# Kernel optimization log

Hardware: AMD Instinct MI355X
Metric: run time of the kernel (lower is better)

Reference implementation:

```python
import jax, jax.numpy as jnp
import numpy as np

Q, N, H, C, L = 512, 1000, 1024, 128, 8  # questions, students, hidden, concepts, lstm layers
LAM, GUESS = 10.0, 0.25  # self.l and guess_prob


def setup_inputs() -> dict:
    key = jax.random.key(0)
    ks = jax.random.split(key, 12)
    def w(k, shape, fan):
        return (jax.random.uniform(k, shape, jnp.float32, -1.0, 1.0) / np.sqrt(fan)).astype(jnp.float32)
    return {
        "inputs": jax.random.normal(ks[0], (Q, N), jnp.float32),
        "concept_col": jax.random.randint(ks[1], (Q,), 0, C),  # concepts[1][i]
        "W_inp": w(ks[2], (H, N), N),
        "b_inp": jnp.zeros((H,), jnp.float32),
        "W_ih0": w(ks[3], (4 * N, H), H),
        "W_hh0": w(ks[4], (4 * N, N), N),
        "b_ih0": jnp.zeros((4 * N,), jnp.float32),
        "b_hh0": jnp.zeros((4 * N,), jnp.float32),
        "W_ih": w(ks[5], (L - 1, 4 * N, N), N),
        "W_hh": w(ks[6], (L - 1, 4 * N, N), N),
        "b_ih": jnp.zeros((L - 1, 4 * N), jnp.float32),
        "b_hh": jnp.zeros((L - 1, 4 * N), jnp.float32),
        "W_lin": w(ks[7], (C,), 1),  # Linear(1, C) weight, shape [C]
        "b_lin": jnp.zeros((C,), jnp.float32),
        "D_nz": 0.1 * jax.random.normal(ks[8], (Q,), jnp.float32),  # D[concepts]
    }


def _cell(Wih, Whh, bih, bhh, x, h, c):
    # PyTorch LSTM cell, gate order i,f,g,o
    g = Wih @ x + bih + Whh @ h + bhh
    i, f, gg, o = jnp.split(g, 4)
    i, f, o = jax.nn.sigmoid(i), jax.nn.sigmoid(f), jax.nn.sigmoid(o)
    c = f * c + i * jnp.tanh(gg)
    return o * jnp.tanh(c), c


def _forward(inputs, concept_col, W_inp, b_inp, W_ih0, W_hh0, b_ih0, b_hh0,
             W_ih, W_hh, b_ih, b_hh, W_lin, b_lin, D_nz):
    def step(carry, xs):
        h, c, ssum = carry  # h,c: [L,N]
        x_row, cc, d = xs
        x = W_inp @ x_row + b_inp  # [H]
        hs, cs = [], []
        hl, cl = _cell(W_ih0, W_hh0, b_ih0, b_hh0, x, h[0], c[0])
        hs.append(hl); cs.append(cl)
        for l in range(L - 1):
            hl, cl = _cell(W_ih[l], W_hh[l], b_ih[l], b_hh[l], hl, h[l + 1], c[l + 1])
            hs.append(hl); cs.append(cl)
        skills = hl[:, None] * W_lin[None, :] + b_lin  # [N, C]
        skills = (skills - skills.min()) / (skills.max() - skills.min())  # global min-max
        out = jnp.maximum(GUESS, 1.0 - jnp.exp(-LAM * (skills[:, cc] - d)))  # floored_exp_irf, [N]
        return (jnp.stack(hs), jnp.stack(cs), ssum + skills), out

    h0 = jnp.zeros((L, N), inputs.dtype)
    c0 = jnp.zeros((L, N), inputs.dtype)
    s0 = jnp.zeros((N, C), inputs.dtype)
    (h, c, ssum), outputs = jax.lax.scan(step, (h0, c0, s0), (inputs, concept_col, D_nz))
    return outputs, ssum / Q  # outputs [Q,N], averaged skills [N,C]


def reference(inputs, concept_col, W_inp, b_inp, W_ih0, W_hh0, b_ih0, b_hh0,
              W_ih, W_hh, b_ih, b_hh, W_lin, b_lin, D_nz):
    return _forward(inputs, concept_col, W_inp, b_inp, W_ih0, W_hh0, b_ih0, b_hh0,
                    W_ih, W_hh, b_ih, b_hh, W_lin, b_lin, D_nz)
```

## Files before the change

kernel.cpp:

```cpp
#include <hip/hip_runtime.h>
#include <math.h>

#define QQ 512
#define NN 1000
#define HHID 1024
#define HPAD 1024
#define CCON 128
#define G4 4000
#define LAYERS 8
#define TC 64
#define CHUNKS (QQ / TC)
#define CONC 4
#define LBLK 63

__device__ inline float wred_min(float v){ for(int o=32;o;o>>=1) v=fminf(v,__shfl_xor(v,o)); return v; }
__device__ inline float wred_max(float v){ for(int o=32;o;o>>=1) v=fmaxf(v,__shfl_xor(v,o)); return v; }
__device__ inline float wred_sum(float v){ for(int o=32;o;o>>=1) v+=__shfl_xor(v,o); return v; }

__global__ __launch_bounds__(256) void gemm_nt(
    const float* __restrict__ A, const float* __restrict__ B,
    const float* __restrict__ bias1,
    float* __restrict__ C, int M, int K, int R, int lda, int ldc) {
  __shared__ float As[16][65];
  __shared__ float Bs[16][65];
  int tid = threadIdx.x;
  int tx = tid & 15, ty = tid >> 4;
  int m0 = blockIdx.y * 64, r0 = blockIdx.x * 64;
  float acc[4][4] = {};
  for (int k0 = 0; k0 < K; k0 += 16) {
#pragma unroll
    for (int i = 0; i < 4; i++) {
      int idx = tid + 256 * i;
      int ml = idx >> 4, kl = idx & 15;
      int m = m0 + ml, k = k0 + kl;
      As[kl][ml] = (m < M && k < K) ? A[(size_t)m * lda + k] : 0.f;
      int r = r0 + ml;
      Bs[kl][ml] = (r < R && k < K) ? B[(size_t)r * K + k] : 0.f;
    }
    __syncthreads();
#pragma unroll
    for (int kk = 0; kk < 16; kk++) {
      float a[4], b[4];
#pragma unroll
      for (int i = 0; i < 4; i++) a[i] = As[kk][ty * 4 + i];
#pragma unroll
      for (int j = 0; j < 4; j++) b[j] = Bs[kk][tx * 4 + j];
#pragma unroll
      for (int i = 0; i < 4; i++)
#pragma unroll
        for (int j = 0; j < 4; j++) acc[i][j] += a[i] * b[j];
    }
    __syncthreads();
  }
#pragma unroll
  for (int i = 0; i < 4; i++) {
    int m = m0 + ty * 4 + i;
    if (m >= M) continue;
#pragma unroll
    for (int j = 0; j < 4; j++) {
      int r = r0 + tx * 4 + j;
      if (r >= R) continue;
      float v = acc[i][j];
      if (bias1) v += bias1[r];
      C[(size_t)m * ldc + r] = v;
    }
  }
}

struct RPair { const float* Hin; const float* Wih; const float* b1;
               const float* b2; const float* Whh; float* Hout; int* flag;
               float* Call; int t0; int kin; };
struct RArgs { RPair p[CONC]; };

__global__ __launch_bounds__(1024, 4) void lstm_stage(RArgs args) {
  RPair rp = args.p[blockIdx.y];
  __shared__ __align__(16) float As[64][68];
  __shared__ __align__(16) float Bs[64][68];
  __shared__ float gl[TC * 64];
  __shared__ float hs[1024];
  __shared__ int go[TC];
  int tid = threadIdx.x;
  int wave = tid >> 6, lane = tid & 63;
  int n = blockIdx.x * 16 + wave;
  bool active = (n < NN);
  int kin = rp.kin;
  int t0 = rp.t0;

  if (tid >= NN) hs[tid] = 0.f;
  if (tid < TC) go[tid] = 0;

  {
    int tt = tid >> 4;
    int w16 = tid & 15;
    int nn = blockIdx.x * 16 + w16;
    float accq[4] = {0.f, 0.f, 0.f, 0.f};
    float pbq[4];
#pragma unroll
    for (int q = 0; q < 4; q++)
      pbq[q] = (nn < NN) ? rp.b1[q * NN + nn] + rp.b2[q * NN + nn] : 0.f;
    for (int k0 = 0; k0 < kin; k0 += 64) {
#pragma unroll
      for (int i = 0; i < 4; i++) {
        int idx = tid + i * 1024;
        int r = idx >> 6, kk = idx & 63;
        int k = k0 + kk;
        As[r][kk] = (k < kin) ? rp.Hin[(size_t)(t0 + r) * HPAD + k] : 0.f;
        int q = r >> 4, nb = blockIdx.x * 16 + (r & 15);
        Bs[r][kk] = (nb < NN && k < kin)
                        ? rp.Wih[(size_t)(q * NN + nb) * kin + k] : 0.f;
      }
      __syncthreads();
#pragma unroll
      for (int kk = 0; kk < 64; kk += 4) {
        float4 av = *(const float4*)&As[tt][kk];
#pragma unroll
        for (int q = 0; q < 4; q++) {
          float4 bv = *(const float4*)&Bs[q * 16 + w16][kk];
          accq[q] += av.x * bv.x + av.y * bv.y + av.z * bv.z + av.w * bv.w;
        }
      }
      __syncthreads();
    }
#pragma unroll
    for (int q = 0; q < 4; q++)
      gl[tt * 64 + q * 16 + w16] = accq[q] + pbq[q];
  }

  float wreg[4][16];
  if (active) {
#pragma unroll
    for (int q = 0; q < 4; q++) {
      const float* wr = rp.Whh + (size_t)(q * NN + n) * NN;
#pragma unroll
      for (int it = 0; it < 16; it++) {
        int k = it * 64 + lane;
        wreg[q][it] = (k < NN) ? wr[k] : 0.f;
      }
    }
  } else {
#pragma unroll
    for (int q = 0; q < 4; q++)
#pragma unroll
      for (int it = 0; it < 16; it++) wreg[q][it] = 0.f;
  }
#pragma unroll
  for (int q = 0; q < 4; q++)
#pragma unroll
    for (int it = 0; it < 16; it++)
      asm volatile("" : "+v"(wreg[q][it]));

  __syncthreads();

  float creg = 0.f;
  if (t0 > 0 && active) creg = rp.Call[n];

  for (int tt = 0; tt < TC; tt++) {
    int t = t0 + tt;
    if (t > 0) {
      if (wave == 0) {
        for (;;) {
          int v = t;
          if (lane < LBLK)
            v = __hip_atomic_load(&rp.flag[lane], __ATOMIC_RELAXED,
                                  __HIP_MEMORY_SCOPE_AGENT);
          if (__all(v >= t)) break;
          __builtin_amdgcn_s_sleep(2);
        }
        if (lane == 0)
          __hip_atomic_store(&go[tt], 1, __ATOMIC_RELAXED,
                             __HIP_MEMORY_SCOPE_WORKGROUP);
      } else {
        while (__hip_atomic_load(&go[tt], __ATOMIC_RELAXED,
                                 __HIP_MEMORY_SCOPE_WORKGROUP) == 0)
          __builtin_amdgcn_s_sleep(1);
      }
      if (tid < NN)
        hs[tid] = __hip_atomic_load(&rp.Hout[(size_t)(t - 1) * HPAD + tid],
                                    __ATOMIC_RELAXED, __HIP_MEMORY_SCOPE_AGENT);
      __syncthreads();
    }
    if (active) {
      float g0 = gl[tt * 64 + wave];
      float g1 = gl[tt * 64 + 16 + wave];
      float g2 = gl[tt * 64 + 32 + wave];
      float g3 = gl[tt * 64 + 48 + wave];
      if (t > 0) {
        float a0 = 0.f, a1 = 0.f, a2 = 0.f, a3 = 0.f;
#pragma unroll
        for (int it = 0; it < 16; it++) {
          float hv = hs[it * 64 + lane];
          a0 += wreg[0][it] * hv;
          a1 += wreg[1][it] * hv;
          a2 += wreg[2][it] * hv;
          a3 += wreg[3][it] * hv;
        }
#pragma unroll
        for (int o = 32; o; o >>= 1) {
          a0 += __shfl_xor(a0, o);
          a1 += __shfl_xor(a1, o);
          a2 += __shfl_xor(a2, o);
          a3 += __shfl_xor(a3, o);
        }
        g0 += a0; g1 += a1; g2 += a2; g3 += a3;
      }
      float ii = 1.f / (1.f + expf(-g0));
      float ff = 1.f / (1.f + expf(-g1));
      float gg = tanhf(g2);
      float oo = 1.f / (1.f + expf(-g3));
      creg = ff * creg + ii * gg;
      float h = oo * tanhf(creg);
      if (lane == 0)
        __hip_atomic_store(&rp.Hout[(size_t)t * HPAD + n], h, __ATOMIC_RELAXED,
                           __HIP_MEMORY_SCOPE_AGENT);
    }
    asm volatile("s_waitcnt vmcnt(0)" ::: "memory");
    __syncthreads();
    if (tid == 0)
      __hip_atomic_store(&rp.flag[blockIdx.x], t + 1, __ATOMIC_RELAXED,
                         __HIP_MEMORY_SCOPE_AGENT);
  }
  if (active && lane == 0)
    __hip_atomic_store(&rp.Call[n], creg, __ATOMIC_RELAXED,
                       __HIP_MEMORY_SCOPE_AGENT);
}

__global__ __launch_bounds__(256) void epilogue_out(
    const float* __restrict__ H7,
    const float* __restrict__ Wlin, const float* __restrict__ blin,
    const int* __restrict__ ccol, const float* __restrict__ Dnz,
    float* __restrict__ out,
    float* __restrict__ irbuf, float* __restrict__ mnirbuf) {
  int t = blockIdx.x, tid = threadIdx.x;
  int wave = tid >> 6, lane = tid & 63;
  __shared__ float hbuf[NN];
  __shared__ float smin[4], smax[4];
  __shared__ float bc[2];
  float lmin = 3.4e38f, lmax = -3.4e38f;
  for (int i = tid; i < NN; i += 256) {
    float v = H7[(size_t)t * HPAD + i];
    hbuf[i] = v;
    lmin = fminf(lmin, v); lmax = fmaxf(lmax, v);
  }
  lmin = wred_min(lmin); lmax = wred_max(lmax);
  if (lane == 0) { smin[wave] = lmin; smax[wave] = lmax; }
  __syncthreads();
  if (tid == 0) {
    bc[0] = fminf(fminf(smin[0], smin[1]), fminf(smin[2], smin[3]));
    bc[1] = fmaxf(fmaxf(smax[0], smax[1]), fmaxf(smax[2], smax[3]));
  }
  __syncthreads();
  float hmn = bc[0], hmx = bc[1];
  float clo = 3.4e38f, chi = -3.4e38f;
  if (tid < CCON) {
    float w = Wlin[tid], b = blin[tid];
    clo = b + fminf(w * hmn, w * hmx);
    chi = b + fmaxf(w * hmn, w * hmx);
  }
  clo = wred_min(clo); chi = wred_max(chi);
  __syncthreads();
  if (lane == 0) { smin[wave] = clo; smax[wave] = chi; }
  __syncthreads();
  if (tid == 0) {
    float mn = fminf(fminf(smin[0], smin[1]), fminf(smin[2], smin[3]));
    float mx = fmaxf(fmaxf(smax[0], smax[1]), fmaxf(smax[2], smax[3]));
    float ir = 1.f / (mx - mn);
    bc[0] = mn; bc[1] = ir;
    irbuf[t] = ir;
    mnirbuf[t] = mn * ir;
  }
  __syncthreads();
  float mn = bc[0], ir = bc[1];
  int cc = ccol[t];
  float wcc = Wlin[cc], bcc = blin[cc], d = Dnz[t];
  for (int n = tid; n < NN; n += 256) {
    float s = (hbuf[n] * wcc + bcc - mn) * ir;
    out[(size_t)t * NN + n] = fmaxf(0.25f, 1.f - expf(-10.f * (s - d)));
  }
}

__global__ void reduce_scalars(const float* __restrict__ ir,
                               const float* __restrict__ mnir,
                               float* __restrict__ scal) {
  int tid = threadIdx.x;
  int wave = tid >> 6, lane = tid & 63;
  __shared__ float s1[8], s2[8];
  float a = ir[tid], b = mnir[tid];
  a = wred_sum(a); b = wred_sum(b);
  if (lane == 0) { s1[wave] = a; s2[wave] = b; }
  __syncthreads();
  if (tid == 0) {
    float A = 0.f, B = 0.f;
    for (int i = 0; i < 8; i++) { A += s1[i]; B += s2[i]; }
    scal[0] = A; scal[1] = B;
  }
}

__global__ void accum_A(const float* __restrict__ H7,
                        const float* __restrict__ ir,
                        float* __restrict__ Avec) {
  int n = blockIdx.x * 256 + threadIdx.x;
  if (n < NN) {
    float acc = 0.f;
    for (int t = 0; t < QQ; t++) acc += H7[(size_t)t * HPAD + n] * ir[t];
    Avec[n] = acc;
  }
}

__global__ void skills_out(const float* __restrict__ Avec,
                           const float* __restrict__ Wlin,
                           const float* __restrict__ blin,
                           const float* __restrict__ scal,
                           float* __restrict__ out) {
  int idx = blockIdx.x * 256 + threadIdx.x;
  if (idx < NN * CCON) {
    int n = idx >> 7, c = idx & 127;
    out[idx] = (Wlin[c] * Avec[n] + blin[c] * scal[0] - scal[1]) * (1.f / (float)QQ);
  }
}

extern "C" void kernel_launch(void* const* d_in, const int* in_sizes, int n_in,
                              void* d_out, int out_size, void* d_ws, size_t ws_size,
                              hipStream_t stream) {
  const float* inputs = (const float*)d_in[0];
  const int*   ccol   = (const int*)d_in[1];
  const float* W_inp  = (const float*)d_in[2];
  const float* b_inp  = (const float*)d_in[3];
  const float* W_ih0  = (const float*)d_in[4];
  const float* W_hh0  = (const float*)d_in[5];
  const float* b_ih0  = (const float*)d_in[6];
  const float* b_hh0  = (const float*)d_in[7];
  const float* W_ih   = (const float*)d_in[8];
  const float* W_hh   = (const float*)d_in[9];
  const float* b_ih   = (const float*)d_in[10];
  const float* b_hh   = (const float*)d_in[11];
  const float* W_lin  = (const float*)d_in[12];
  const float* b_lin  = (const float*)d_in[13];
  const float* D_nz   = (const float*)d_in[14];

  float* ws = (float*)d_ws;
  float* X    = ws;
  float* H    = X + (size_t)QQ * HPAD;
  float* Call = H + (size_t)LAYERS * QQ * HPAD;
  float* irb  = Call + LAYERS * HPAD;
  float* mnir = irb + QQ;
  float* Avec = mnir + QQ;
  float* scal = Avec + 1024;
  int*   flags = (int*)(scal + 16);

  float* out_main   = (float*)d_out;
  float* out_skills = (float*)d_out + QQ * NN;

  hipMemsetAsync(flags, 0, LAYERS * 64 * sizeof(int), stream);

  gemm_nt<<<dim3(HPAD / 64, QQ / 64), 256, 0, stream>>>(
      inputs, W_inp, b_inp, X, QQ, NN, HPAD, NN, HPAD);

  bool donep[LAYERS][CHUNKS] = {};
  int remaining = LAYERS * CHUNKS;
  while (remaining > 0) {
    int pl[CONC], pcid[CONC];
    bool sel[LAYERS][CHUNKS] = {};
    int np = 0;
    for (int pick = 0; pick < CONC; pick++) {
      int bl = -1, bc = -1, bkey = 1 << 30;
      for (int l = 0; l < LAYERS; l++)
        for (int c = 0; c < CHUNKS; c++) {
          if (donep[l][c] || sel[l][c]) continue;
          if (l > 0 && !donep[l - 1][c]) continue;
          if (c > 0 && !donep[l][c - 1]) continue;
          int key = (l + c) * 16 + (LAYERS - 1 - l);
          if (key < bkey) { bkey = key; bl = l; bc = c; }
        }
      if (bl < 0) break;
      sel[bl][bc] = true; pl[np] = bl; pcid[np] = bc; np++;
    }
    RArgs ra;
    for (int i = 0; i < np; i++) {
      int l = pl[i], c = pcid[i];
      RPair& r = ra.p[i];
      if (l == 0) {
        r.Hin = X; r.Wih = W_ih0; r.b1 = b_ih0; r.b2 = b_hh0;
        r.Whh = W_hh0; r.kin = HHID;
      } else {
        r.Hin = H + (size_t)(l - 1) * QQ * HPAD;
        r.Wih = W_ih + (size_t)(l - 1) * G4 * NN;
        r.b1 = b_ih + (size_t)(l - 1) * G4;
        r.b2 = b_hh + (size_t)(l - 1) * G4;
        r.Whh = W_hh + (size_t)(l - 1) * G4 * NN;
        r.kin = NN;
      }
      r.Hout = H + (size_t)l * QQ * HPAD;
      r.flag = flags + l * 64;
      r.Call = Call + l * HPAD;
      r.t0 = c * TC;
    }
    for (int i = np; i < CONC; i++) ra.p[i] = ra.p[0];
    lstm_stage<<<dim3(LBLK, np), 1024, 0, stream>>>(ra);
    for (int i = 0; i < np; i++) donep[pl[i]][pcid[i]] = true;
    remaining -= np;
  }

  float* H7 = H + (size_t)7 * QQ * HPAD;
  epilogue_out<<<QQ, 256, 0, stream>>>(H7, W_lin, b_lin, ccol, D_nz,
                                       out_main, irb, mnir);
  reduce_scalars<<<1, 512, 0, stream>>>(irb, mnir, scal);
  accum_A<<<4, 256, 0, stream>>>(H7, irb, Avec);
  skills_out<<<(NN * CCON) / 256, 256, 0, stream>>>(Avec, W_lin, b_lin, scal,
                                                    out_skills);
}
```

Before: 7.962 ms.

## Replace host-scheduled wavefront launches with one persistent layer-pipelined LSTM kernel

Replaces the host-side wavefront scheduler, which issued many lstm_stage launches covering up to four (layer, chunk) pairs each, with a single persistent kernel. That kernel runs all 8 layers at once, with 125 blocks of 512 threads per layer. Each layer waits on per-block progress flags from the previous layer before computing a chunk's input projection, then steps through timesteps using intra-layer flag barriers. Recurrent weights stay in registers across all chunks, which removes the Call state save/restore and the repeated launches and weight reloads. The design relies on all 1000 blocks being co-resident, since inter-block spin-waits can deadlock if the GPU cannot hold them all. Each block now covers 8 rather than 16 units, which raises the number of blocks polling the flags.

```diff
diff --git a/kernel.cpp b/kernel.cpp
--- a/kernel.cpp
+++ b/kernel.cpp
@@ -10,8 +10,7 @@
 #define LAYERS 8
 #define TC 64
 #define CHUNKS (QQ / TC)
-#define CONC 4
-#define LBLK 63
+#define LB 125
 
 __device__ inline float wred_min(float v){ for(int o=32;o;o>>=1) v=fminf(v,__shfl_xor(v,o)); return v; }
 __device__ inline float wred_max(float v){ for(int o=32;o;o>>=1) v=fmaxf(v,__shfl_xor(v,o)); return v; }
@@ -67,161 +66,209 @@
   }
 }
 
-struct RPair { const float* Hin; const float* Wih; const float* b1;
-               const float* b2; const float* Whh; float* Hout; int* flag;
-               float* Call; int t0; int kin; };
-struct RArgs { RPair p[CONC]; };
-
-__global__ __launch_bounds__(1024, 4) void lstm_stage(RArgs args) {
-  RPair rp = args.p[blockIdx.y];
-  __shared__ __align__(16) float As[64][68];
-  __shared__ __align__(16) float Bs[64][68];
-  __shared__ float gl[TC * 64];
+struct PipeArgs {
+  const float* X;
+  const float* Wih0; const float* Whh0;
+  const float* bih0; const float* bhh0;
+  const float* Wih; const float* Whh;
+  const float* bih; const float* bhh;
+  float* H;
+  int* flags;
+};
+
+__global__ __launch_bounds__(512, 4) void lstm_pipe(PipeArgs a) {
+  int layer = blockIdx.x / LB;
+  int blk = blockIdx.x - layer * LB;
+  __shared__ float As[64][65];
+  __shared__ float Bs[32][65];
+  __shared__ float gl[TC * 32];
   __shared__ float hs[1024];
   __shared__ int go[TC];
+  __shared__ int goC;
   int tid = threadIdx.x;
   int wave = tid >> 6, lane = tid & 63;
-  int n = blockIdx.x * 16 + wave;
-  bool active = (n < NN);
-  int kin = rp.kin;
-  int t0 = rp.t0;
-
-  if (tid >= NN) hs[tid] = 0.f;
+  int n = blk * 8 + wave;
+
+  int kin = (layer == 0) ? HHID : NN;
+  const float* WihL = (layer == 0) ? a.Wih0 : a.Wih + (size_t)(layer - 1) * G4 * NN;
+  const float* WhhL = (layer == 0) ? a.Whh0 : a.Whh + (size_t)(layer - 1) * G4 * NN;
+  const float* b1 = (layer == 0) ? a.bih0 : a.bih + (size_t)(layer - 1) * G4;
+  const float* b2 = (layer == 0) ? a.bhh0 : a.bhh + (size_t)(layer - 1) * G4;
+  const float* Hin = (layer == 0) ? a.X : a.H + (size_t)(layer - 1) * QQ * HPAD;
+  float* Hout = a.H + (size_t)layer * QQ * HPAD;
+  int* fown = a.flags + layer * 128;
+  int* fprev = a.flags + (layer - 1) * 128;
+
+  if (tid >= 488) hs[512 + tid] = 0.f;
   if (tid < TC) go[tid] = 0;
-
-  {
-    int tt = tid >> 4;
-    int w16 = tid & 15;
-    int nn = blockIdx.x * 16 + w16;
-    float accq[4] = {0.f, 0.f, 0.f, 0.f};
-    float pbq[4];
-#pragma unroll
-    for (int q = 0; q < 4; q++)
-      pbq[q] = (nn < NN) ? rp.b1[q * NN + nn] + rp.b2[q * NN + nn] : 0.f;
-    for (int k0 = 0; k0 < kin; k0 += 64) {
-#pragma unroll
-      for (int i = 0; i < 4; i++) {
-        int idx = tid + i * 1024;
-        int r = idx >> 6, kk = idx & 63;
-        int k = k0 + kk;
-        As[r][kk] = (k < kin) ? rp.Hin[(size_t)(t0 + r) * HPAD + k] : 0.f;
-        int q = r >> 4, nb = blockIdx.x * 16 + (r & 15);
-        Bs[r][kk] = (nb < NN && k < kin)
-                        ? rp.Wih[(size_t)(q * NN + nb) * kin + k] : 0.f;
+  if (tid == 0) goC = 0;
+
+  float wreg[4][16];
+#pragma unroll
+  for (int q = 0; q < 4; q++) {
+    const float* wr = WhhL + (size_t)(q * NN + n) * NN;
+#pragma unroll
+    for (int it = 0; it < 16; it++) {
+      int k = it * 64 + lane;
+      wreg[q][it] = (k < NN) ? wr[k] : 0.f;
+    }
+  }
+#pragma unroll
+  for (int q = 0; q < 4; q++)
+#pragma unroll
+    for (int it = 0; it < 16; it++)
+      asm volatile("" : "+v"(wreg[q][it]));
+
+  int w8 = tid & 7, ttA = tid >> 3;
+  int nbA = blk * 8 + w8;
+  float pbA[4];
+#pragma unroll
+  for (int q = 0; q < 4; q++)
+    pbA[q] = b1[q * NN + nbA] + b2[q * NN + nbA];
+
+  __syncthreads();
+
+  float creg = 0.f;
+
+  for (int c = 0; c < CHUNKS; c++) {
+    int t0 = c * TC;
+    if (layer > 0) {
+      int need = t0 + TC;
+      if (wave == 0) {
+        for (;;) {
+          int ok = 1;
+          if (lane < LB)
+            ok &= (__hip_atomic_load(&fprev[lane], __ATOMIC_RELAXED,
+                                     __HIP_MEMORY_SCOPE_AGENT) >= need);
+          if (lane < LB - 64)
+            ok &= (__hip_atomic_load(&fprev[64 + lane], __ATOMIC_RELAXED,
+                                     __HIP_MEMORY_SCOPE_AGENT) >= need);
+          if (__all(ok)) break;
+          __builtin_amdgcn_s_sleep(4);
+        }
+        if (lane == 0)
+          __hip_atomic_store(&goC, c + 1, __ATOMIC_RELAXED,
+                             __HIP_MEMORY_SCOPE_WORKGROUP);
+      } else {
+        while (__hip_atomic_load(&goC, __ATOMIC_RELAXED,
+                                 __HIP_MEMORY_SCOPE_WORKGROUP) < c + 1)
+          __builtin_amdgcn_s_sleep(2);
       }
       __syncthreads();
-#pragma unroll
-      for (int kk = 0; kk < 64; kk += 4) {
-        float4 av = *(const float4*)&As[tt][kk];
-#pragma unroll
-        for (int q = 0; q < 4; q++) {
-          float4 bv = *(const float4*)&Bs[q * 16 + w16][kk];
-          accq[q] += av.x * bv.x + av.y * bv.y + av.z * bv.z + av.w * bv.w;
-        }
+    }
+    {
+      float accq[4] = {0.f, 0.f, 0.f, 0.f};
+      for (int k0 = 0; k0 < kin; k0 += 64) {
+#pragma unroll
+        for (int i = 0; i < 8; i++) {
+          int idx = tid + i * 512;
+          int r = idx >> 6, kk = idx & 63;
+          int k = k0 + kk;
+          As[r][kk] = (k < kin)
+              ? __hip_atomic_load(&Hin[(size_t)(t0 + r) * HPAD + k],
+                                  __ATOMIC_RELAXED, __HIP_MEMORY_SCOPE_AGENT)
+              : 0.f;
+        }
+#pragma unroll
+        for (int i = 0; i < 4; i++) {
+          int idx = tid + i * 512;
+          int r = idx >> 6, kk = idx & 63;
+          int k = k0 + kk;
+          int q = r >> 3, nb = blk * 8 + (r & 7);
+          Bs[r][kk] = (k < kin) ? WihL[(size_t)(q * NN + nb) * kin + k] : 0.f;
+        }
+        __syncthreads();
+#pragma unroll
+        for (int kk = 0; kk < 64; kk++) {
+          float av = As[ttA][kk];
+          accq[0] += av * Bs[w8][kk];
+          accq[1] += av * Bs[8 + w8][kk];
+          accq[2] += av * Bs[16 + w8][kk];
+          accq[3] += av * Bs[24 + w8][kk];
+        }
+        __syncthreads();
       }
+#pragma unroll
+      for (int q = 0; q < 4; q++)
+        gl[ttA * 32 + q * 8 + w8] = accq[q] + pbA[q];
+    }
+    __syncthreads();
+
+    for (int tt = 0; tt < TC; tt++) {
+      int t = t0 + tt;
+      if (t > 0) {
+        if (wave == 0) {
+          for (;;) {
+            int ok = 1;
+            if (lane < LB)
+              ok &= (__hip_atomic_load(&fown[lane], __ATOMIC_RELAXED,
+                                       __HIP_MEMORY_SCOPE_AGENT) >= t);
+            if (lane < LB - 64)
+              ok &= (__hip_atomic_load(&fown[64 + lane], __ATOMIC_RELAXED,
+                                       __HIP_MEMORY_SCOPE_AGENT) >= t);
+            if (__all(ok)) break;
+            __builtin_amdgcn_s_sleep(2);
+          }
+          if (lane == 0)
+            __hip_atomic_store(&go[tt], t, __ATOMIC_RELAXED,
+                               __HIP_MEMORY_SCOPE_WORKGROUP);
+        } else {
+          while (__hip_atomic_load(&go[tt], __ATOMIC_RELAXED,
+                                   __HIP_MEMORY_SCOPE_WORKGROUP) < t)
+            __builtin_amdgcn_s_sleep(1);
+        }
+        if (tid < NN)
+          hs[tid] = __hip_atomic_load(&Hout[(size_t)(t - 1) * HPAD + tid],
+                                      __ATOMIC_RELAXED, __HIP_MEMORY_SCOPE_AGENT);
+        {
+          int i2 = tid + 512;
+          if (i2 < NN)
+            hs[i2] = __hip_atomic_load(&Hout[(size_t)(t - 1) * HPAD + i2],
+                                       __ATOMIC_RELAXED, __HIP_MEMORY_SCOPE_AGENT);
+        }
+        __syncthreads();
+      }
+      {
+        float g0 = gl[tt * 32 + wave];
+        float g1 = gl[tt * 32 + 8 + wave];
+        float g2 = gl[tt * 32 + 16 + wave];
+        float g3 = gl[tt * 32 + 24 + wave];
+        if (t > 0) {
+          float a0 = 0.f, a1 = 0.f, a2 = 0.f, a3 = 0.f;
+#pragma unroll
+          for (int it = 0; it < 16; it++) {
+            float hv = hs[it * 64 + lane];
+            a0 += wreg[0][it] * hv;
+            a1 += wreg[1][it] * hv;
+            a2 += wreg[2][it] * hv;
+            a3 += wreg[3][it] * hv;
+          }
+#pragma unroll
+          for (int o = 32; o; o >>= 1) {
+            a0 += __shfl_xor(a0, o);
+            a1 += __shfl_xor(a1, o);
+            a2 += __shfl_xor(a2, o);
+            a3 += __shfl_xor(a3, o);
+          }
+          g0 += a0; g1 += a1; g2 += a2; g3 += a3;
+        }
+        float ii = 1.f / (1.f + expf(-g0));
+        float ff = 1.f / (1.f + expf(-g1));
+        float gg = tanhf(g2);
+        float oo = 1.f / (1.f + expf(-g3));
+        creg = ff * creg + ii * gg;
+        float h = oo * tanhf(creg);
+        if (lane == 0)
+          __hip_atomic_store(&Hout[(size_t)t * HPAD + n], h, __ATOMIC_RELAXED,
+                             __HIP_MEMORY_SCOPE_AGENT);
+      }
+      asm volatile("s_waitcnt vmcnt(0)" ::: "memory");
       __syncthreads();
-    }
-#pragma unroll
-    for (int q = 0; q < 4; q++)
-      gl[tt * 64 + q * 16 + w16] = accq[q] + pbq[q];
-  }
-
-  float wreg[4][16];
-  if (active) {
-#pragma unroll
-    for (int q = 0; q < 4; q++) {
-      const float* wr = rp.Whh + (size_t)(q * NN + n) * NN;
-#pragma unroll
-      for (int it = 0; it < 16; it++) {
-        int k = it * 64 + lane;
-        wreg[q][it] = (k < NN) ? wr[k] : 0.f;
-      }
-    }
-  } else {
-#pragma unroll
-    for (int q = 0; q < 4; q++)
-#pragma unroll
-      for (int it = 0; it < 16; it++) wreg[q][it] = 0.f;
-  }
-#pragma unroll
-  for (int q = 0; q < 4; q++)
-#pragma unroll
-    for (int it = 0; it < 16; it++)
-      asm volatile("" : "+v"(wreg[q][it]));
-
-  __syncthreads();
-
-  float creg = 0.f;
-  if (t0 > 0 && active) creg = rp.Call[n];
-
-  for (int tt = 0; tt < TC; tt++) {
-    int t = t0 + tt;
-    if (t > 0) {
-      if (wave == 0) {
-        for (;;) {
-          int v = t;
-          if (lane < LBLK)
-            v = __hip_atomic_load(&rp.flag[lane], __ATOMIC_RELAXED,
-                                  __HIP_MEMORY_SCOPE_AGENT);
-          if (__all(v >= t)) break;
-          __builtin_amdgcn_s_sleep(2);
-        }
-        if (lane == 0)
-          __hip_atomic_store(&go[tt], 1, __ATOMIC_RELAXED,
-                             __HIP_MEMORY_SCOPE_WORKGROUP);
-      } else {
-        while (__hip_atomic_load(&go[tt], __ATOMIC_RELAXED,
-                                 __HIP_MEMORY_SCOPE_WORKGROUP) == 0)
-          __builtin_amdgcn_s_sleep(1);
-      }
-      if (tid < NN)
-        hs[tid] = __hip_atomic_load(&rp.Hout[(size_t)(t - 1) * HPAD + tid],
-                                    __ATOMIC_RELAXED, __HIP_MEMORY_SCOPE_AGENT);
-      __syncthreads();
-    }
-    if (active) {
-      float g0 = gl[tt * 64 + wave];
-      float g1 = gl[tt * 64 + 16 + wave];
-      float g2 = gl[tt * 64 + 32 + wave];
-      float g3 = gl[tt * 64 + 48 + wave];
-      if (t > 0) {
-        float a0 = 0.f, a1 = 0.f, a2 = 0.f, a3 = 0.f;
-#pragma unroll
-        for (int it = 0; it < 16; it++) {
-          float hv = hs[it * 64 + lane];
-          a0 += wreg[0][it] * hv;
-          a1 += wreg[1][it] * hv;
-          a2 += wreg[2][it] * hv;
-          a3 += wreg[3][it] * hv;
-        }
-#pragma unroll
-        for (int o = 32; o; o >>= 1) {
-          a0 += __shfl_xor(a0, o);
-          a1 += __shfl_xor(a1, o);
-          a2 += __shfl_xor(a2, o);
-          a3 += __shfl_xor(a3, o);
-        }
-        g0 += a0; g1 += a1; g2 += a2; g3 += a3;
-      }
-      float ii = 1.f / (1.f + expf(-g0));
-      float ff = 1.f / (1.f + expf(-g1));
-      float gg = tanhf(g2);
-      float oo = 1.f / (1.f + expf(-g3));
-      creg = ff * creg + ii * gg;
-      float h = oo * tanhf(creg);
-      if (lane == 0)
-        __hip_atomic_store(&rp.Hout[(size_t)t * HPAD + n], h, __ATOMIC_RELAXED,
+      if (tid == 0)
+        __hip_atomic_store(&fown[blk], t + 1, __ATOMIC_RELAXED,
                            __HIP_MEMORY_SCOPE_AGENT);
     }
-    asm volatile("s_waitcnt vmcnt(0)" ::: "memory");
-    __syncthreads();
-    if (tid == 0)
-      __hip_atomic_store(&rp.flag[blockIdx.x], t + 1, __ATOMIC_RELAXED,
-                         __HIP_MEMORY_SCOPE_AGENT);
-  }
-  if (active && lane == 0)
-    __hip_atomic_store(&rp.Call[n], creg, __ATOMIC_RELAXED,
-                       __HIP_MEMORY_SCOPE_AGENT);
+  }
 }
 
 __global__ __launch_bounds__(256) void epilogue_out(
@@ -340,8 +387,7 @@
   float* ws = (float*)d_ws;
   float* X    = ws;
   float* H    = X + (size_t)QQ * HPAD;
-  float* Call = H + (size_t)LAYERS * QQ * HPAD;
-  float* irb  = Call + LAYERS * HPAD;
+  float* irb  = H + (size_t)LAYERS * QQ * HPAD;
   float* mnir = irb + QQ;
   float* Avec = mnir + QQ;
   float* scal = Avec + 1024;
@@ -350,55 +396,16 @@
   float* out_main   = (float*)d_out;
   float* out_skills = (float*)d_out + QQ * NN;
 
-  hipMemsetAsync(flags, 0, LAYERS * 64 * sizeof(int), stream);
+  hipMemsetAsync(flags, 0, LAYERS * 128 * sizeof(int), stream);
 
   gemm_nt<<<dim3(HPAD / 64, QQ / 64), 256, 0, stream>>>(
       inputs, W_inp, b_inp, X, QQ, NN, HPAD, NN, HPAD);
 
-  bool donep[LAYERS][CHUNKS] = {};
-  int remaining = LAYERS * CHUNKS;
-  while (remaining > 0) {
-    int pl[CONC], pcid[CONC];
-    bool sel[LAYERS][CHUNKS] = {};
-    int np = 0;
-    for (int pick = 0; pick < CONC; pick++) {
-      int bl = -1, bc = -1, bkey = 1 << 30;
-      for (int l = 0; l < LAYERS; l++)
-        for (int c = 0; c < CHUNKS; c++) {
-          if (donep[l][c] || sel[l][c]) continue;
-          if (l > 0 && !donep[l - 1][c]) continue;
-          if (c > 0 && !donep[l][c - 1]) continue;
-          int key = (l + c) * 16 + (LAYERS - 1 - l);
-          if (key < bkey) { bkey = key; bl = l; bc = c; }
-        }
-      if (bl < 0) break;
-      sel[bl][bc] = true; pl[np] = bl; pcid[np] = bc; np++;
-    }
-    RArgs ra;
-    for (int i = 0; i < np; i++) {
-      int l = pl[i], c = pcid[i];
-      RPair& r = ra.p[i];
-      if (l == 0) {
-        r.Hin = X; r.Wih = W_ih0; r.b1 = b_ih0; r.b2 = b_hh0;
-        r.Whh = W_hh0; r.kin = HHID;
-      } else {
-        r.Hin = H + (size_t)(l - 1) * QQ * HPAD;
-        r.Wih = W_ih + (size_t)(l - 1) * G4 * NN;
-        r.b1 = b_ih + (size_t)(l - 1) * G4;
-        r.b2 = b_hh + (size_t)(l - 1) * G4;
-        r.Whh = W_hh + (size_t)(l - 1) * G4 * NN;
-        r.kin = NN;
-      }
-      r.Hout = H + (size_t)l * QQ * HPAD;
-      r.flag = flags + l * 64;
-      r.Call = Call + l * HPAD;
-      r.t0 = c * TC;
-    }
-    for (int i = np; i < CONC; i++) ra.p[i] = ra.p[0];
-    lstm_stage<<<dim3(LBLK, np), 1024, 0, stream>>>(ra);
-    for (int i = 0; i < np; i++) donep[pl[i]][pcid[i]] = true;
-    remaining -= np;
-  }
+  PipeArgs pa;
+  pa.X = X; pa.Wih0 = W_ih0; pa.Whh0 = W_hh0; pa.bih0 = b_ih0; pa.bhh0 = b_hh0;
+  pa.Wih = W_ih; pa.Whh = W_hh; pa.bih = b_ih; pa.bhh = b_hh;
+  pa.H = H; pa.flags = flags;
+  lstm_pipe<<<LAYERS * LB, 512, 0, stream>>>(pa);
 
   float* H7 = H + (size_t)7 * QQ * HPAD;
   epilogue_out<<<QQ, 256, 0, stream>>>(H7, W_lin, b_lin, ccol, D_nz,
```

Measured after the change: 13.25 ms. 66.5% more time.
